# Kernel optimization log

Measured on AMD Instinct MI355X. Metric: run time of the kernel, lower is better.

## Reference

```python
import jax, jax.numpy as jnp
import numpy as np

B, K, N, T, C = 2, 2, 4096, 8, 3
H = 192            # hidden_dim
NODE_DIM = 10
N_LAYERS = 10
KNN = 16           # k nearest neighbours
TOP_FRAC = 0.4
SHARP = 5.0        # mask_sharpness
S = max(int(TOP_FRAC * N), KNN + 1)   # n_select per graph


def _ln(x, g, b, eps=1e-5):
    mu = x.mean(-1, keepdims=True)
    v = ((x - mu) ** 2).mean(-1, keepdims=True)  # biased var, matches nn.LayerNorm
    return (x - mu) / jnp.sqrt(v + eps) * g + b


def setup_inputs() -> dict:
    key = jax.random.key(0)
    ks = jax.random.split(key, 12)
    rn = lambda k, shape: 0.05 * jax.random.normal(k, shape, jnp.float32)
    F0 = 2 * NODE_DIM + 4   # first EdgeConv MLP in-dim
    FR = 2 * H + 4          # remaining EdgeConv MLP in-dim
    L = N_LAYERS - 1
    return {
        "u_base": jax.random.normal(ks[0], (B, K, N, C), jnp.float32),
        "pos": jax.random.uniform(ks[1], (B, N, 3), dtype=jnp.float32),
        "velocity_in": jax.random.normal(ks[2], (B, T, N, C), jnp.float32),
        "airfoil_mask": (jax.random.uniform(ks[3], (B, N)) < 0.05).astype(jnp.float32),
        "conv0_w1": rn(ks[4], (F0, H)), "conv0_b1": jnp.zeros((H,)),
        "conv0_w2": rn(ks[5], (H, H)), "conv0_b2": jnp.zeros((H,)),
        "conv0_g": jnp.ones((H,)), "conv0_be": jnp.zeros((H,)),
        "convs_w1": rn(ks[6], (L, FR, H)), "convs_b1": jnp.zeros((L, H)),
        "convs_w2": rn(ks[7], (L, H, H)), "convs_b2": jnp.zeros((L, H)),
        "convs_g": jnp.ones((L, H)), "convs_be": jnp.zeros((L, H)),
        "head_g": jnp.ones((H,)), "head_be": jnp.zeros((H,)),
        "head_w1": rn(ks[8], (H, H)), "head_b1": jnp.zeros((H,)),
        "head_w2": rn(ks[9], (H, 3)), "head_b2": jnp.zeros((3,)),
    }


def reference(u_base, pos, velocity_in, airfoil_mask,
              conv0_w1, conv0_b1, conv0_w2, conv0_b2, conv0_g, conv0_be,
              convs_w1, convs_b1, convs_w2, convs_b2, convs_g, convs_be,
              head_g, head_be, head_w1, head_b1, head_w2, head_b2):
    # --- variance gating (torch .var/.std are unbiased) ---
    var_pp = jnp.var(velocity_in, axis=1, ddof=1).sum(-1)                      # [B,N]
    var_z = (var_pp - var_pp.mean(1, keepdims=True)) / (
        jnp.std(var_pp, axis=1, ddof=1, keepdims=True) + 1e-8)
    soft_mask = jax.nn.sigmoid(SHARP * var_z) * (1.0 - airfoil_mask)           # [B,N]

    # --- select top-variance points per graph ---
    _, top_idx = jax.lax.top_k(var_pp, S)                                      # [B,S]
    pos_sel = jnp.take_along_axis(pos, top_idx[..., None], axis=1)             # [B,S,3]
    mask_sel = jnp.take_along_axis(soft_mask, top_idx, axis=1)[..., None]      # [B,S,1]
    v_last = velocity_in[:, -1]                                                # [B,N,C]
    ub_sel = jnp.take_along_axis(u_base, top_idx[:, None, :, None], axis=2)    # [B,K,S,C]
    vl_sel = jnp.take_along_axis(v_last, top_idx[..., None], axis=1)           # [B,S,C]
    vf_sel = jnp.take_along_axis(var_pp[..., None], top_idx[..., None], axis=1)
    static = jnp.concatenate([vl_sel, pos_sel, vf_sel], -1)                    # [B,S,7]
    x0 = jnp.concatenate(
        [ub_sel, jnp.broadcast_to(static[:, None], (B, K, S, 7))], -1)         # [B,K,S,10]

    def per_graph(x, pos_b):  # x: [K,S,F0], pos_b: [S,3]
        # kNN graph (self excluded via +inf diagonal, as in the chunked cdist)
        d2 = jnp.sum((pos_b[:, None] - pos_b[None]) ** 2, -1)                  # [S,S]
        d2 = d2.at[jnp.arange(S), jnp.arange(S)].set(jnp.inf)
        _, knn = jax.lax.top_k(-d2, KNN)                                       # [S,KNN]
        # PyG convention with edge_index=stack([targets, sources]):
        # i = edge_index[1] = knn neighbours, j = edge_index[0] = centre nodes
        idx_i = knn.reshape(-1)                     # [E] aggregation targets
        idx_j = jnp.repeat(jnp.arange(S), KNN)      # [E]
        rel = pos_b[idx_i] - pos_b[idx_j]           # pos[edge_index[1]] - pos[edge_index[0]]
        dist = jnp.linalg.norm(rel, axis=-1, keepdims=True)
        ea = jnp.concatenate([rel, dist], -1)       # [E,4]
        ea_b = jnp.broadcast_to(ea, (K,) + ea.shape)

        def conv(h, w1, b1, w2, b2, g, be):
            hi = h[:, idx_i]
            hj = h[:, idx_j]
            m = jnp.concatenate([hi, hj - hi, ea_b], -1)                       # [K,E,2F+4]
            m = jax.nn.gelu(m @ w1 + b1, approximate=False) @ w2 + b2          # [K,E,H]
            agg = jnp.zeros((K, S, H), h.dtype).at[:, idx_i].add(m)
            return _ln(agg, g, be)

        h = conv(x, conv0_w1, conv0_b1, conv0_w2, conv0_b2, conv0_g, conv0_be)
        for l in range(N_LAYERS - 1):
            h = conv(h, convs_w1[l], convs_b1[l], convs_w2[l], convs_b2[l],
                     convs_g[l], convs_be[l]) + h
        hh = _ln(h, head_g, head_be)
        return jax.nn.gelu(hh @ head_w1 + head_b1, approximate=False) @ head_w2 + head_b2

    delta = jax.vmap(per_graph)(x0, pos_sel)        # [B,K,S,3]
    delta = delta * mask_sel[:, None]               # [B,1,S,1]

    def scatter_b(idx, d):  # idx [S], d [K,S,3]
        return jnp.zeros((K, N, C), d.dtype).at[:, idx].set(d)

    delta_full = jax.vmap(scatter_b)(top_idx, delta)            # [B,K,N,C]
    return (u_base + delta_full) * (1.0 - airfoil_mask)[:, None, :, None]
```

## Files before the change

kernel.cpp:

```cpp
#include <hip/hip_runtime.h>
#include <hip/hip_bf16.h>
#include <math.h>

#define B_ 2
#define K_ 2
#define NN_ 4096
#define T_ 8
#define C_ 3
#define H_ 192
#define S_ 1638
#define KK_ 16
#define E_ (S_*KK_)
#define NROW (B_*K_*S_)
#define SHARP_ 5.0f

typedef __hip_bfloat16 bf;
typedef unsigned long long ull;
typedef __bf16 bf16x8 __attribute__((ext_vector_type(8)));
typedef float f32x4 __attribute__((ext_vector_type(4)));

__device__ int   g_isbf16;
__device__ __align__(16) float g_var[B_*NN_];
__device__ __align__(16) float g_vs1[B_*16];
__device__ __align__(16) float g_vs2[B_*16];
__device__ __align__(16) int   g_topidx[B_*S_];
__device__ __align__(16) float g_possel[B_*S_*3];
__device__ __align__(16) float g_masksel[B_*S_];
__device__ __align__(16) float g_x0[NROW*10];
__device__ __align__(16) int   g_knn[B_*E_];
__device__ __align__(16) float g_ea[B_*E_*4];
__device__ __align__(16) int   g_indeg[B_*S_];
__device__ __align__(16) int   g_cursor[B_*S_];
__device__ __align__(16) int   g_off[B_*(S_+1)];
__device__ __align__(16) int   g_list[B_*E_];
__device__ __align__(16) float g_P[(size_t)NROW*H_];
__device__ __align__(16) bf    g_Qbf[(size_t)NROW*H_];
__device__ __align__(16) float g_h[(size_t)NROW*H_];
__device__ __align__(16) bf    g_abf[(size_t)NROW*H_];
__device__ __align__(16) bf    g_w2p[(size_t)11*H_*H_];
__device__ __align__(16) bf    g_wcp[(size_t)9*H_*384];

__device__ __forceinline__ float bf2f(bf x){ return __bfloat162float(x); }
__device__ __forceinline__ float LD(const void* p, long i){
  return g_isbf16 ? __bfloat162float(((const bf*)p)[i]) : ((const float*)p)[i];
}
__device__ __forceinline__ float LDi(const void* p, long i, int isb){
  return isb ? __bfloat162float(((const bf*)p)[i]) : ((const float*)p)[i];
}
__device__ __forceinline__ float gelu_f(float x){ return 0.5f*x*(1.0f + erff(x*0.70710678118654752f)); }
__device__ __forceinline__ ull shfl_xor_u64(ull v, int m){
  unsigned lo = (unsigned)v, hi = (unsigned)(v >> 32);
  lo = __shfl_xor(lo, m, 64); hi = __shfl_xor(hi, m, 64);
  return ((ull)hi << 32) | lo;
}

__global__ __launch_bounds__(256) void k_var(const void* __restrict__ vel,
                                             const void* __restrict__ ub,
                                             const void* __restrict__ pos){
  __shared__ int s_bad;
  int b = blockIdx.y;
  int bx = blockIdx.x;
  int tid = threadIdx.x;
  if (tid == 0) s_bad = 0;
  __syncthreads();
  {
    const bf* pa = (const bf*)ub; const bf* pb = (const bf*)pos; const bf* pc = (const bf*)vel;
    int bad = 0;
    #pragma unroll
    for (int s = 0; s < 2; ++s){
      float va = __bfloat162float(pa[tid + s*256]);
      float vb = __bfloat162float(pb[tid + s*256]);
      float vc = __bfloat162float(pc[tid + s*256]);
      if (!(fabsf(va) <= 1000.f)) bad = 1;
      if (!(fabsf(vb) <= 1000.f)) bad = 1;
      if (!(fabsf(vc) <= 1000.f)) bad = 1;
    }
    if (bad) atomicOr(&s_bad, 1);
  }
  __syncthreads();
  int isb = (s_bad == 0) ? 1 : 0;
  if (bx == 0 && b == 0 && tid == 0) g_isbf16 = isb;
  int zi = (b*16 + bx)*256 + tid;
  if (zi < B_*S_){ g_indeg[zi] = 0; g_cursor[zi] = 0; }
  int n = bx*256 + tid;
  float v = 0.f;
  #pragma unroll
  for (int c = 0; c < 3; ++c){
    float x[8];
    #pragma unroll
    for (int t = 0; t < 8; ++t)
      x[t] = LDi(vel, ((long)(b*T_+t)*NN_ + n)*3 + c, isb);
    float m = __fadd_rn(__fadd_rn(__fadd_rn(x[0],x[1]), __fadd_rn(x[2],x[3])),
                        __fadd_rn(__fadd_rn(x[4],x[5]), __fadd_rn(x[6],x[7]))) / 8.0f;
    float d[8];
    #pragma unroll
    for (int t = 0; t < 8; ++t){ float dd = __fadd_rn(x[t], -m); d[t] = __fmul_rn(dd,dd); }
    float sv = __fadd_rn(__fadd_rn(__fadd_rn(d[0],d[1]), __fadd_rn(d[2],d[3])),
                         __fadd_rn(__fadd_rn(d[4],d[5]), __fadd_rn(d[6],d[7])));
    v = __fadd_rn(v, sv / 7.0f);
  }
  g_var[b*NN_ + n] = v;
  float s1 = v, s2 = v*v;
  #pragma unroll
  for (int o = 32; o; o >>= 1){ s1 += __shfl_xor(s1,o,64); s2 += __shfl_xor(s2,o,64); }
  __shared__ float r1[4], r2[4];
  int lane = tid & 63, wid = tid >> 6;
  if (!lane){ r1[wid]=s1; r2[wid]=s2; }
  __syncthreads();
  if (tid == 0){
    g_vs1[b*16 + bx] = r1[0]+r1[1]+r1[2]+r1[3];
    g_vs2[b*16 + bx] = r2[0]+r2[1]+r2[2]+r2[3];
  }
}

__global__ __launch_bounds__(256) void k_rank(){
  int b = blockIdx.y;
  int i = blockIdx.x*4 + (threadIdx.x >> 6);
  int lane = threadIdx.x & 63;
  float vi = g_var[b*NN_+i];
  int rank = 0;
  for (int j = lane; j < NN_; j += 64){
    float vj = g_var[b*NN_+j];
    rank += ((vj > vi) || (vj == vi && j < i)) ? 1 : 0;
  }
  #pragma unroll
  for (int o = 32; o; o >>= 1) rank += __shfl_xor(rank, o, 64);
  if (lane == 0 && rank < S_) g_topidx[b*S_ + rank] = i;
}

__global__ void k_gather(const void* __restrict__ pos, const void* __restrict__ ub,
                         const void* __restrict__ vel, const void* __restrict__ air){
  int gi = blockIdx.x*256 + threadIdx.x;
  if (gi >= B_*S_) return;
  int b = gi / S_, s = gi - b*S_;
  int node = g_topidx[gi];
  float px = LD(pos, ((long)b*NN_+node)*3+0);
  float py = LD(pos, ((long)b*NN_+node)*3+1);
  float pz = LD(pos, ((long)b*NN_+node)*3+2);
  g_possel[gi*3+0]=px; g_possel[gi*3+1]=py; g_possel[gi*3+2]=pz;
  float S1 = 0.f, S2 = 0.f;
  #pragma unroll
  for (int t = 0; t < 16; ++t){ S1 += g_vs1[b*16+t]; S2 += g_vs2[b*16+t]; }
  float mean = S1*(1.f/NN_);
  float sd = sqrtf(fmaxf((S2 - S1*S1*(1.f/NN_))*(1.f/(NN_-1)), 0.f));
  float vf = g_var[b*NN_+node];
  float z = (vf-mean)/(sd+1e-8f);
  float sig = 1.f/(1.f+expf(-SHARP_*z));
  g_masksel[gi] = sig*(1.f - LD(air, b*NN_+node));
  float vl0 = LD(vel, ((long)(b*T_+7)*NN_+node)*3+0);
  float vl1 = LD(vel, ((long)(b*T_+7)*NN_+node)*3+1);
  float vl2 = LD(vel, ((long)(b*T_+7)*NN_+node)*3+2);
  for (int k = 0; k < K_; ++k){
    long row = (long)(b*K_+k)*S_ + s;
    float* x = g_x0 + row*10;
    x[0]=LD(ub, ((long)(b*K_+k)*NN_+node)*3+0);
    x[1]=LD(ub, ((long)(b*K_+k)*NN_+node)*3+1);
    x[2]=LD(ub, ((long)(b*K_+k)*NN_+node)*3+2);
    x[3]=vl0; x[4]=vl1; x[5]=vl2;
    x[6]=px;  x[7]=py;  x[8]=pz;
    x[9]=vf;
  }
}

__global__ __launch_bounds__(256) void k_knn(){
  __shared__ float px[S_], py[S_], pz[S_];
  int b = blockIdx.y;
  int j = blockIdx.x*4 + (threadIdx.x >> 6);
  int lane = threadIdx.x & 63;
  for (int t = threadIdx.x; t < S_; t += 256){
    px[t] = g_possel[(b*S_+t)*3+0];
    py[t] = g_possel[(b*S_+t)*3+1];
    pz[t] = g_possel[(b*S_+t)*3+2];
  }
  __syncthreads();
  if (j >= S_) return;
  float xj=px[j], yj=py[j], zj=pz[j];
  float dist[KK_]; int id[KK_];
  #pragma unroll
  for (int t = 0; t < KK_; ++t){ dist[t]=3.0e38f; id[t]=0x7fffffff; }
  for (int c = lane; c < S_; c += 64){
    if (c == j) continue;
    float dx=__fadd_rn(px[c],-xj), dy=__fadd_rn(py[c],-yj), dz=__fadd_rn(pz[c],-zj);
    float d2 = __fadd_rn(__fadd_rn(__fmul_rn(dx,dx), __fmul_rn(dy,dy)), __fmul_rn(dz,dz));
    if (d2 < dist[KK_-1]){
      int p = 0;
      #pragma unroll
      for (int q = 0; q < KK_; ++q) p += (dist[q] <= d2) ? 1 : 0;
      #pragma unroll
      for (int q = KK_-1; q >= 1; --q){
        bool mv = (q > p);
        dist[q] = mv ? dist[q-1] : dist[q];
        id[q]   = mv ? id[q-1]   : id[q];
      }
      #pragma unroll
      for (int q = 0; q < KK_; ++q){ if (q == p){ dist[q] = d2; id[q] = c; } }
    }
  }
  ull mykey = 0;
  #pragma unroll
  for (int t = 0; t < KK_; ++t){
    ull k = (((ull)__float_as_uint(dist[0])) << 32) | (unsigned)id[0];
    ull m = k;
    #pragma unroll
    for (int o = 32; o; o >>= 1){ ull other = shfl_xor_u64(m, o); m = (other < m) ? other : m; }
    if (k == m){
      #pragma unroll
      for (int q = 0; q < KK_-1; ++q){ dist[q]=dist[q+1]; id[q]=id[q+1]; }
      dist[KK_-1] = 3.0e38f; id[KK_-1] = 0x7fffffff;
    }
    if (lane == t) mykey = m;
  }
  if (lane < KK_){
    int i = (int)(mykey & 0xffffffffu);
    g_knn[(b*S_+j)*KK_ + lane] = i;
    float rx = __fadd_rn(px[i],-xj), ry = __fadd_rn(py[i],-yj), rz = __fadd_rn(pz[i],-zj);
    float dd = sqrtf(__fadd_rn(__fadd_rn(__fmul_rn(rx,rx), __fmul_rn(ry,ry)), __fmul_rn(rz,rz)));
    float* o = g_ea + ((long)b*E_ + j*KK_ + lane)*4;
    o[0]=rx; o[1]=ry; o[2]=rz; o[3]=dd;
    atomicAdd(&g_indeg[b*S_+i], 1);
  }
}

__global__ void k_scan(){
  __shared__ int sA[2048], sB[2048];
  int b = blockIdx.x, tid = threadIdx.x;
  for (int i = tid; i < 2048; i += 1024) sA[i] = (i < S_) ? g_indeg[b*S_+i] : 0;
  __syncthreads();
  int *src = sA, *dst = sB;
  for (int d = 1; d < 2048; d <<= 1){
    for (int i = tid; i < 2048; i += 1024) dst[i] = src[i] + (i >= d ? src[i-d] : 0);
    __syncthreads();
    int* t2 = src; src = dst; dst = t2;
  }
  if (tid == 0) g_off[b*(S_+1)] = 0;
  for (int i = tid; i < S_; i += 1024) g_off[b*(S_+1)+i+1] = src[i];
}

__global__ void k_fill(){
  int idx = blockIdx.x*256 + threadIdx.x;
  if (idx >= B_*E_) return;
  int b = idx / E_, e = idx - b*E_;
  int i = g_knn[idx];
  int slot = atomicAdd(&g_cursor[b*S_+i], 1);
  g_list[b*E_ + g_off[b*(S_+1)+i] + slot] = e;
}

#define PW2_BLKS 1584
#define PWC_BLKS 2592
#define INIT_BLKS 192
__global__ void k_packall(const void* __restrict__ c0w2, const void* __restrict__ cw2,
                          const void* __restrict__ hw1, const void* __restrict__ cw1,
                          const void* __restrict__ ub, const void* __restrict__ air,
                          float* __restrict__ out){
  int blk = blockIdx.x;
  if (blk < PW2_BLKS){
    int gi = blk*256 + threadIdx.x;
    if (gi >= 11*H_*H_) return;
    int mat = gi / (H_*H_), r = gi - mat*(H_*H_);
    int k = r / H_, n = r - (r/H_)*H_;
    float v;
    if (mat == 0)      v = LD(c0w2, (long)k*H_ + n);
    else if (mat <= 9) v = LD(cw2, (long)(mat-1)*H_*H_ + (long)k*H_ + n);
    else               v = LD(hw1, (long)k*H_ + n);
    int t = k>>5, q = (k>>3)&3, jj = k&7;
    g_w2p[(size_t)mat*H_*H_ + (((t*4+q)*H_ + n)*8 + jj)] = __float2bfloat16(v);
  } else if (blk < PW2_BLKS + PWC_BLKS){
    int gi = (blk - PW2_BLKS)*256 + threadIdx.x;
    if (gi >= 9*H_*384) return;
    int l = gi / (H_*384), r = gi - l*(H_*384);
    int k = r / 384, n = r - (r/384)*384;
    long base = (long)l*388*H_;
    float v;
    if (n < H_) v = LD(cw1, base + (long)k*H_ + n) - LD(cw1, base + (long)(H_+k)*H_ + n);
    else        v = LD(cw1, base + (long)(H_+k)*H_ + (n-H_));
    int t = k>>5, q = (k>>3)&3, jj = k&7;
    g_wcp[(size_t)l*(H_*384) + (((t*4+q)*384 + n)*8 + jj)] = __float2bfloat16(v);
  } else {
    int gi = (blk - PW2_BLKS - PWC_BLKS)*256 + threadIdx.x;
    int n = (gi/3) % NN_;
    int b = gi / (K_*NN_*C_);
    float a = 1.f - LD(air, b*NN_+n);
    out[gi] = LD(ub, gi) * a;
  }
}

__global__ __launch_bounds__(256) void k_proj0(const void* __restrict__ w1){
  __shared__ float xs[16][10];
  __shared__ float wP[10][192];
  __shared__ float wQ[10][192];
  int tid = threadIdx.x;
  long rowBase = (long)blockIdx.x * 16;
  for (int idx = tid; idx < 1920; idx += 256){
    int f = idx / 192, n = idx - (idx/192)*192;
    float a = LD(w1, f*H_+n), b = LD(w1, (10+f)*H_+n);
    wP[f][n] = a - b; wQ[f][n] = b;
  }
  for (int idx = tid; idx < 160; idx += 256){
    int r = idx / 10, f = idx - (idx/10)*10;
    long row = rowBase + r; if (row >= NROW) row = NROW-1;
    xs[r][f] = g_x0[row*10 + f];
  }
  __syncthreads();
  for (int o = tid; o < 16*384; o += 256){
    int r = o / 384, n = o - (o/384)*384;
    long row = rowBase + r;
    if (row >= NROW) continue;
    float acc = 0.f;
    if (n < 192){
      #pragma unroll
      for (int f = 0; f < 10; ++f) acc += xs[r][f]*wP[f][n];
      g_P[row*192 + n] = acc;
    } else {
      int nc = n - 192;
      #pragma unroll
      for (int f = 0; f < 10; ++f) acc += xs[r][f]*wQ[f][nc];
      g_Qbf[row*192 + nc] = __float2bfloat16(acc);
    }
  }
}

template<int RES, int DOPQ>
__global__ __launch_bounds__(256) void k_lnpq(const void* __restrict__ biasB, long biasO,
                                              const void* __restrict__ gB, long gO,
                                              const void* __restrict__ beB, long beO,
                                              int bOff, int pqOff, int M){
  const bf* A  = g_abf;
  const bf* Bp = g_w2p + bOff;
  int wave = threadIdx.x >> 6, lane = threadIdx.x & 63;
  int q = lane >> 4, l16 = lane & 15;
  long rowBase = (long)blockIdx.x * 16;
  f32x4 acc[3];
  #pragma unroll
  for (int ct = 0; ct < 3; ++ct) acc[ct] = (f32x4){0.f,0.f,0.f,0.f};
  #pragma unroll
  for (int t = 0; t < 6; ++t){
    int kof = t*32 + q*8;
    long r = rowBase + l16; if (r >= M) r = M-1;
    bf16x8 af = *reinterpret_cast<const bf16x8*>(A + r*192 + kof);
    #pragma unroll
    for (int ct = 0; ct < 3; ++ct){
      int n = wave*48 + ct*16 + l16;
      bf16x8 bfr = *reinterpret_cast<const bf16x8*>(Bp + (((t*4+q)*192 + n)*8));
      acc[ct] = __builtin_amdgcn_mfma_f32_16x16x32_bf16(af, bfr, acc[ct], 0,0,0);
    }
  }
  __shared__ float tile[16][200];
  __shared__ bf    ybf[16][200];
  __shared__ float srow[16], rrow[16];
  #pragma unroll
  for (int ct = 0; ct < 3; ++ct){
    int col = wave*48 + ct*16 + l16;
    float bb = LD(biasB, biasO + col);
    #pragma unroll
    for (int r = 0; r < 4; ++r){
      int lr = q*4 + r;
      long row = rowBase + lr;
      long rowc = (row < M) ? row : (M-1);
      int bk = (int)(rowc / S_); int i = (int)(rowc - (long)bk*S_); int b = bk >> 1;
      float degf = (float)(g_off[b*(S_+1)+i+1] - g_off[b*(S_+1)+i]);
      tile[lr][col] = acc[ct][r] + degf*bb;
    }
  }
  __syncthreads();
  {
    int lr = threadIdx.x >> 4;
    int k16 = threadIdx.x & 15;
    float s = 0.f, qq = 0.f;
    for (int c = k16; c < 192; c += 16){ float x = tile[lr][c]; s += x; qq += x*x; }
    #pragma unroll
    for (int o = 1; o < 16; o <<= 1){ s += __shfl_xor(s,o,64); qq += __shfl_xor(qq,o,64); }
    if (k16 == 0){
      float mu = s*(1.f/H_);
      float var = qq*(1.f/H_) - mu*mu;
      srow[lr] = mu;
      rrow[lr] = rsqrtf(fmaxf(var, 0.f) + 1e-5f);
    }
  }
  __syncthreads();
  for (int o = threadIdx.x; o < 16*192; o += 256){
    int lr = o / 192, col = o - (o/192)*192;
    long row = rowBase + lr;
    long rowc = (row < M) ? row : (M-1);
    float y = (tile[lr][col] - srow[lr])*rrow[lr]*LD(gB,gO+col) + LD(beB,beO+col);
    if (RES) y += g_h[rowc*192 + col];
    if (row < M) g_h[row*192 + col] = y;
    ybf[lr][col] = __float2bfloat16(y);
  }
  if (DOPQ){
    __syncthreads();
    const bf* Bq = g_wcp + pqOff;
    f32x4 acc2[6];
    #pragma unroll
    for (int ct = 0; ct < 6; ++ct) acc2[ct] = (f32x4){0.f,0.f,0.f,0.f};
    #pragma unroll
    for (int t = 0; t < 6; ++t){
      int kof = t*32 + q*8;
      bf16x8 af = *reinterpret_cast<const bf16x8*>(&ybf[l16][kof]);
      #pragma unroll
      for (int ct = 0; ct < 6; ++ct){
        int n = wave*96 + ct*16 + l16;
        bf16x8 bfr = *reinterpret_cast<const bf16x8*>(Bq + (((t*4+q)*384 + n)*8));
        acc2[ct] = __builtin_amdgcn_mfma_f32_16x16x32_bf16(af, bfr, acc2[ct], 0,0,0);
      }
    }
    #pragma unroll
    for (int ct = 0; ct < 6; ++ct){
      int col = wave*96 + ct*16 + l16;
      #pragma unroll
      for (int r = 0; r < 4; ++r){
        long row = rowBase + q*4 + r;
        if (row < M){
          float v = acc2[ct][r];
          if (col < 192) g_P[row*192 + col] = v;
          else           g_Qbf[row*192 + (col-192)] = __float2bfloat16(v);
        }
      }
    }
  }
}

__global__ __launch_bounds__(256) void k_head(const void* __restrict__ gB,
                                              const void* __restrict__ beB,
                                              const void* __restrict__ biasB,
                                              const void* __restrict__ w2,
                                              const void* __restrict__ b2,
                                              const void* __restrict__ ubase,
                                              const void* __restrict__ air,
                                              float* __restrict__ out,
                                              int bOff, int M){
  const bf* Bp = g_w2p + bOff;
  int wave = threadIdx.x >> 6, lane = threadIdx.x & 63;
  int q = lane >> 4, l16 = lane & 15;
  long rowBase = (long)blockIdx.x * 32;
  __shared__ float tile[32][200];
  __shared__ bf hb_s[32][216];
  __shared__ float srow[32], rrow[32];
  for (int o = threadIdx.x; o < 32*192; o += 256){
    int lr = o / 192, col = o - (o/192)*192;
    long row = rowBase + lr;
    long rowc = (row < M) ? row : (M-1);
    tile[lr][col] = g_h[rowc*192 + col];
  }
  __syncthreads();
  {
    int lr = threadIdx.x >> 3;
    int k8 = threadIdx.x & 7;
    float s = 0.f, qq = 0.f;
    for (int c = k8; c < 192; c += 8){ float x = tile[lr][c]; s += x; qq += x*x; }
    #pragma unroll
    for (int o = 1; o < 8; o <<= 1){ s += __shfl_xor(s,o,64); qq += __shfl_xor(qq,o,64); }
    if (k8 == 0){
      float mu = s*(1.f/H_);
      float var = qq*(1.f/H_) - mu*mu;
      srow[lr] = mu;
      rrow[lr] = rsqrtf(fmaxf(var, 0.f) + 1e-5f);
    }
  }
  __syncthreads();
  for (int o = threadIdx.x; o < 32*192; o += 256){
    int lr = o / 192, col = o - (o/192)*192;
    hb_s[lr][col] = __float2bfloat16((tile[lr][col] - srow[lr])*rrow[lr]*LD(gB,col) + LD(beB,col));
  }
  __syncthreads();
  f32x4 acc[2][3];
  #pragma unroll
  for (int rt = 0; rt < 2; ++rt)
    #pragma unroll
    for (int ct = 0; ct < 3; ++ct) acc[rt][ct] = (f32x4){0.f,0.f,0.f,0.f};
  #pragma unroll
  for (int t = 0; t < 6; ++t){
    int kof = t*32 + q*8;
    bf16x8 af[2], bfr[3];
    #pragma unroll
    for (int rt = 0; rt < 2; ++rt)
      af[rt] = *reinterpret_cast<const bf16x8*>(&hb_s[rt*16 + l16][kof]);
    #pragma unroll
    for (int ct = 0; ct < 3; ++ct){
      int n = wave*48 + ct*16 + l16;
      bfr[ct] = *reinterpret_cast<const bf16x8*>(Bp + (((t*4+q)*192 + n)*8));
    }
    #pragma unroll
    for (int rt = 0; rt < 2; ++rt)
      #pragma unroll
      for (int ct = 0; ct < 3; ++ct)
        acc[rt][ct] = __builtin_amdgcn_mfma_f32_16x16x32_bf16(af[rt], bfr[ct], acc[rt][ct], 0,0,0);
  }
  #pragma unroll
  for (int rt = 0; rt < 2; ++rt){
    #pragma unroll
    for (int ct = 0; ct < 3; ++ct){
      int col = wave*48 + ct*16 + l16;
      float bb = LD(biasB, col);
      #pragma unroll
      for (int r = 0; r < 4; ++r){
        int lr = rt*16 + q*4 + r;
        tile[lr][col] = gelu_f(acc[rt][ct][r] + bb);
      }
    }
  }
  __syncthreads();
  {
    int r = threadIdx.x >> 3, k8 = threadIdx.x & 7;
    long row = rowBase + r;
    float p0 = 0.f, p1 = 0.f, p2 = 0.f;
    for (int col = k8; col < 192; col += 8){
      float tv = tile[r][col];
      p0 += tv*LD(w2, col*3+0);
      p1 += tv*LD(w2, col*3+1);
      p2 += tv*LD(w2, col*3+2);
    }
    #pragma unroll
    for (int o = 1; o < 8; o <<= 1){
      p0 += __shfl_xor(p0,o,64);
      p1 += __shfl_xor(p1,o,64);
      p2 += __shfl_xor(p2,o,64);
    }
    if (k8 == 0 && row < M){
      int bk = (int)(row / S_), s = (int)(row - (long)bk*S_), b = bk >> 1;
      float msk = g_masksel[b*S_+s];
      int node = g_topidx[b*S_+s];
      float am = 1.f - LD(air, b*NN_+node);
      float d0 = p0 + LD(b2,0), d1 = p1 + LD(b2,1), d2 = p2 + LD(b2,2);
      long oi = ((long)bk*NN_ + node)*3;
      out[oi+0] = (LD(ubase, oi+0) + d0*msk)*am;
      out[oi+1] = (LD(ubase, oi+1) + d1*msk)*am;
      out[oi+2] = (LD(ubase, oi+2) + d2*msk)*am;
    }
  }
}

__global__ __launch_bounds__(192) void k_aggedge(const void* __restrict__ w1cB, long w1cO,
                                                 const void* __restrict__ b1B, long b1O){
  int row = blockIdx.x;
  int col = threadIdx.x;
  int bk = row / S_, i = row - bk*S_, b = bk >> 1;
  int off = g_off[b*(S_+1)+i];
  int deg = g_off[b*(S_+1)+i+1] - off;
  float w0 = LD(w1cB, w1cO+col),       w1v = LD(w1cB, w1cO+H_+col);
  float w2v = LD(w1cB, w1cO+2*H_+col), w3v = LD(w1cB, w1cO+3*H_+col);
  float base = g_P[(size_t)row*H_ + col] + LD(b1B, b1O+col);
  const int* lst = g_list + b*E_ + off;
  const bf* Q = g_Qbf + (size_t)bk*S_*H_;
  const float* EA = g_ea + (size_t)b*E_*4;
  float acc = 0.f;
  int d = 0;
  for (; d + 4 <= deg; d += 4){
    int e0 = lst[d], e1 = lst[d+1], e2 = lst[d+2], e3 = lst[d+3];
    float4 a0 = *reinterpret_cast<const float4*>(EA + (size_t)e0*4);
    float4 a1 = *reinterpret_cast<const float4*>(EA + (size_t)e1*4);
    float4 a2 = *reinterpret_cast<const float4*>(EA + (size_t)e2*4);
    float4 a3 = *reinterpret_cast<const float4*>(EA + (size_t)e3*4);
    float q0 = bf2f(Q[(size_t)(e0>>4)*H_ + col]);
    float q1 = bf2f(Q[(size_t)(e1>>4)*H_ + col]);
    float q2 = bf2f(Q[(size_t)(e2>>4)*H_ + col]);
    float q3 = bf2f(Q[(size_t)(e3>>4)*H_ + col]);
    acc += gelu_f(base + q0 + a0.x*w0 + a0.y*w1v + a0.z*w2v + a0.w*w3v);
    acc += gelu_f(base + q1 + a1.x*w0 + a1.y*w1v + a1.z*w2v + a1.w*w3v);
    acc += gelu_f(base + q2 + a2.x*w0 + a2.y*w1v + a2.z*w2v + a2.w*w3v);
    acc += gelu_f(base + q3 + a3.x*w0 + a3.y*w1v + a3.z*w2v + a3.w*w3v);
  }
  for (; d < deg; ++d){
    int e = lst[d];
    float4 a = *reinterpret_cast<const float4*>(EA + (size_t)e*4);
    float qv = bf2f(Q[(size_t)(e>>4)*H_ + col]);
    acc += gelu_f(base + qv + a.x*w0 + a.y*w1v + a.z*w2v + a.w*w3v);
  }
  g_abf[(size_t)row*H_ + col] = __float2bfloat16(acc);
}

extern "C" void kernel_launch(void* const* d_in, const int* in_sizes, int n_in,
                              void* d_out, int out_size, void* d_ws, size_t ws_size,
                              hipStream_t stream) {
  (void)in_sizes; (void)n_in; (void)d_ws; (void)ws_size; (void)out_size;
  const void* u_base = d_in[0];
  const void* pos    = d_in[1];
  const void* vel    = d_in[2];
  const void* air    = d_in[3];
  const void* c0w1   = d_in[4];
  const void* c0b1   = d_in[5];
  const void* c0w2   = d_in[6];
  const void* c0b2   = d_in[7];
  const void* c0g    = d_in[8];
  const void* c0be   = d_in[9];
  const void* cw1    = d_in[10];
  const void* cb1    = d_in[11];
  const void* cw2    = d_in[12];
  const void* cb2    = d_in[13];
  const void* cg     = d_in[14];
  const void* cbe    = d_in[15];
  const void* hg     = d_in[16];
  const void* hbe    = d_in[17];
  const void* hw1    = d_in[18];
  const void* hb1    = d_in[19];
  const void* hw2    = d_in[20];
  const void* hb2    = d_in[21];
  float* out = (float*)d_out;

  k_var<<<dim3(16, B_), 256, 0, stream>>>(vel, u_base, pos);
  k_rank<<<dim3(NN_/4, B_), 256, 0, stream>>>();
  k_gather<<<13, 256, 0, stream>>>(pos, u_base, vel, air);
  k_knn<<<dim3((S_+3)/4, B_), 256, 0, stream>>>();
  k_scan<<<B_, 1024, 0, stream>>>();
  k_fill<<<205, 256, 0, stream>>>();
  k_packall<<<PW2_BLKS + PWC_BLKS + INIT_BLKS, 256, 0, stream>>>(c0w2, cw2, hw1, cw1, u_base, air, out);
  k_proj0<<<410, 256, 0, stream>>>(c0w1);

  const int GN16 = (NROW + 15) / 16;
  for (int l = 0; l < 10; ++l){
    long w1cO = (l == 0) ? 20L*H_ : ((long)(l-1)*388 + 384)*H_;
    const void* w1cB = (l == 0) ? c0w1 : cw1;
    long lOff = (l == 0) ? 0 : (long)(l-1)*H_;
    const void* b1B = (l == 0) ? c0b1 : cb1;
    k_aggedge<<<NROW, 192, 0, stream>>>(w1cB, w1cO, b1B, lOff);

    const void* b2B = (l == 0) ? c0b2 : cb2;
    const void* gB  = (l == 0) ? c0g  : cg;
    const void* beB = (l == 0) ? c0be : cbe;
    if (l == 0)
      k_lnpq<0,1><<<GN16, 256, 0, stream>>>(b2B, lOff, gB, lOff, beB, lOff, 0,        0,         NROW);
    else if (l < 9)
      k_lnpq<1,1><<<GN16, 256, 0, stream>>>(b2B, lOff, gB, lOff, beB, lOff, l*H_*H_, l*H_*384,  NROW);
    else
      k_lnpq<1,0><<<GN16, 256, 0, stream>>>(b2B, lOff, gB, lOff, beB, lOff, l*H_*H_, 0,         NROW);
  }

  k_head<<<(NROW + 31)/32, 256, 0, stream>>>(hg, hbe, hb1, hw2, hb2, u_base, air, out, 10*H_*H_, NROW);
}
```

Measured before the change: 617.8 us.

## Fuse edge aggregation, projection, LayerNorm and head into one per-layer kernel

The per-row edge aggregation is merged into the per-layer MFMA/LayerNorm/PQ kernel. Aggregated activations now stay in shared memory as bf16 instead of going through the global g_abf buffer, and the head runs inside the last layer's kernel. The k_fill and k_proj0 setup kernels are folded into the packing kernel, so there are fewer launches and less global traffic. In exchange each block handles only 8 rows but pads them to a 16-row MFMA tile, so half of the matrix work is spent on zeros. The gather-heavy aggregation also now runs on far fewer, larger blocks, which may lower latency hiding.

```diff
diff --git a/kernel.cpp b/kernel.cpp
--- a/kernel.cpp
+++ b/kernel.cpp
@@ -36,7 +36,6 @@
 __device__ __align__(16) float g_P[(size_t)NROW*H_];
 __device__ __align__(16) bf    g_Qbf[(size_t)NROW*H_];
 __device__ __align__(16) float g_h[(size_t)NROW*H_];
-__device__ __align__(16) bf    g_abf[(size_t)NROW*H_];
 __device__ __align__(16) bf    g_w2p[(size_t)11*H_*H_];
 __device__ __align__(16) bf    g_wcp[(size_t)9*H_*384];
 
@@ -236,22 +235,15 @@
   for (int i = tid; i < S_; i += 1024) g_off[b*(S_+1)+i+1] = src[i];
 }
 
-__global__ void k_fill(){
-  int idx = blockIdx.x*256 + threadIdx.x;
-  if (idx >= B_*E_) return;
-  int b = idx / E_, e = idx - b*E_;
-  int i = g_knn[idx];
-  int slot = atomicAdd(&g_cursor[b*S_+i], 1);
-  g_list[b*E_ + g_off[b*(S_+1)+i] + slot] = e;
-}
-
 #define PW2_BLKS 1584
 #define PWC_BLKS 2592
 #define INIT_BLKS 192
+#define FILL_BLKS 205
+#define PROJ_BLKS 410
 __global__ void k_packall(const void* __restrict__ c0w2, const void* __restrict__ cw2,
                           const void* __restrict__ hw1, const void* __restrict__ cw1,
                           const void* __restrict__ ub, const void* __restrict__ air,
-                          float* __restrict__ out){
+                          float* __restrict__ out, const void* __restrict__ c0w1){
   int blk = blockIdx.x;
   if (blk < PW2_BLKS){
     int gi = blk*256 + threadIdx.x;
@@ -275,90 +267,143 @@
     else        v = LD(cw1, base + (long)(H_+k)*H_ + (n-H_));
     int t = k>>5, q = (k>>3)&3, jj = k&7;
     g_wcp[(size_t)l*(H_*384) + (((t*4+q)*384 + n)*8 + jj)] = __float2bfloat16(v);
-  } else {
+  } else if (blk < PW2_BLKS + PWC_BLKS + INIT_BLKS){
     int gi = (blk - PW2_BLKS - PWC_BLKS)*256 + threadIdx.x;
     int n = (gi/3) % NN_;
     int b = gi / (K_*NN_*C_);
     float a = 1.f - LD(air, b*NN_+n);
     out[gi] = LD(ub, gi) * a;
-  }
-}
-
-__global__ __launch_bounds__(256) void k_proj0(const void* __restrict__ w1){
-  __shared__ float xs[16][10];
-  __shared__ float wP[10][192];
-  __shared__ float wQ[10][192];
-  int tid = threadIdx.x;
-  long rowBase = (long)blockIdx.x * 16;
-  for (int idx = tid; idx < 1920; idx += 256){
-    int f = idx / 192, n = idx - (idx/192)*192;
-    float a = LD(w1, f*H_+n), b = LD(w1, (10+f)*H_+n);
-    wP[f][n] = a - b; wQ[f][n] = b;
-  }
-  for (int idx = tid; idx < 160; idx += 256){
-    int r = idx / 10, f = idx - (idx/10)*10;
-    long row = rowBase + r; if (row >= NROW) row = NROW-1;
-    xs[r][f] = g_x0[row*10 + f];
-  }
-  __syncthreads();
-  for (int o = tid; o < 16*384; o += 256){
-    int r = o / 384, n = o - (o/384)*384;
-    long row = rowBase + r;
-    if (row >= NROW) continue;
-    float acc = 0.f;
-    if (n < 192){
-      #pragma unroll
-      for (int f = 0; f < 10; ++f) acc += xs[r][f]*wP[f][n];
-      g_P[row*192 + n] = acc;
-    } else {
-      int nc = n - 192;
-      #pragma unroll
-      for (int f = 0; f < 10; ++f) acc += xs[r][f]*wQ[f][nc];
-      g_Qbf[row*192 + nc] = __float2bfloat16(acc);
-    }
-  }
-}
-
-template<int RES, int DOPQ>
-__global__ __launch_bounds__(256) void k_lnpq(const void* __restrict__ biasB, long biasO,
-                                              const void* __restrict__ gB, long gO,
-                                              const void* __restrict__ beB, long beO,
-                                              int bOff, int pqOff, int M){
-  const bf* A  = g_abf;
-  const bf* Bp = g_w2p + bOff;
+  } else if (blk < PW2_BLKS + PWC_BLKS + INIT_BLKS + FILL_BLKS){
+    int idx = (blk - PW2_BLKS - PWC_BLKS - INIT_BLKS)*256 + threadIdx.x;
+    if (idx >= B_*E_) return;
+    int b = idx / E_, e = idx - b*E_;
+    int i = g_knn[idx];
+    int slot = atomicAdd(&g_cursor[b*S_+i], 1);
+    g_list[b*E_ + g_off[b*(S_+1)+i] + slot] = e;
+  } else {
+    __shared__ float xs[16][10];
+    __shared__ float wP[10][192];
+    __shared__ float wQ[10][192];
+    int tid = threadIdx.x;
+    long rowBase = (long)(blk - PW2_BLKS - PWC_BLKS - INIT_BLKS - FILL_BLKS) * 16;
+    for (int idx = tid; idx < 1920; idx += 256){
+      int f = idx / 192, n = idx - (idx/192)*192;
+      float a = LD(c0w1, f*H_+n), b = LD(c0w1, (10+f)*H_+n);
+      wP[f][n] = a - b; wQ[f][n] = b;
+    }
+    for (int idx = tid; idx < 160; idx += 256){
+      int r = idx / 10, f = idx - (idx/10)*10;
+      long row = rowBase + r; if (row >= NROW) row = NROW-1;
+      xs[r][f] = g_x0[row*10 + f];
+    }
+    __syncthreads();
+    for (int o = tid; o < 16*384; o += 256){
+      int r = o / 384, n = o - (o/384)*384;
+      long row = rowBase + r;
+      if (row >= NROW) continue;
+      float acc = 0.f;
+      if (n < 192){
+        #pragma unroll
+        for (int f = 0; f < 10; ++f) acc += xs[r][f]*wP[f][n];
+        g_P[row*192 + n] = acc;
+      } else {
+        int nc = n - 192;
+        #pragma unroll
+        for (int f = 0; f < 10; ++f) acc += xs[r][f]*wQ[f][nc];
+        g_Qbf[row*192 + nc] = __float2bfloat16(acc);
+      }
+    }
+  }
+}
+
+template<int RES, int DOPQ, int DOHEAD>
+__global__ __launch_bounds__(256) void k_layer(
+    const void* __restrict__ w1cB, long w1cO,
+    const void* __restrict__ b1B, long b1O,
+    const void* __restrict__ biasB, long biasO,
+    const void* __restrict__ gB, long gO,
+    const void* __restrict__ beB, long beO,
+    int bOff, int pqOff,
+    const void* __restrict__ hg, const void* __restrict__ hbe,
+    const void* __restrict__ hb1, const void* __restrict__ hw2,
+    const void* __restrict__ hb2, const void* __restrict__ ubase,
+    const void* __restrict__ air, float* __restrict__ out,
+    int M){
   int wave = threadIdx.x >> 6, lane = threadIdx.x & 63;
   int q = lane >> 4, l16 = lane & 15;
-  long rowBase = (long)blockIdx.x * 16;
-  f32x4 acc[3];
-  #pragma unroll
-  for (int ct = 0; ct < 3; ++ct) acc[ct] = (f32x4){0.f,0.f,0.f,0.f};
-  #pragma unroll
-  for (int t = 0; t < 6; ++t){
-    int kof = t*32 + q*8;
-    long r = rowBase + l16; if (r >= M) r = M-1;
-    bf16x8 af = *reinterpret_cast<const bf16x8*>(A + r*192 + kof);
+  long rowBase = (long)blockIdx.x * 8;
+  __shared__ bf    sbf[16][200];
+  __shared__ float tile[16][200];
+  __shared__ float srow[16], rrow[16];
+  for (int o = threadIdx.x; o < 8*192; o += 256){
+    int lr = o / 192, col = o - (o/192)*192;
+    long row = rowBase + lr;
+    int bk = (int)(row / S_); int i = (int)(row - (long)bk*S_); int b = bk >> 1;
+    int off = g_off[b*(S_+1)+i];
+    int deg = g_off[b*(S_+1)+i+1] - off;
+    float w0 = LD(w1cB, w1cO+col),       w1v = LD(w1cB, w1cO+H_+col);
+    float w2v = LD(w1cB, w1cO+2*H_+col), w3v = LD(w1cB, w1cO+3*H_+col);
+    float base = g_P[(size_t)row*H_ + col] + LD(b1B, b1O+col);
+    const int* lst = g_list + b*E_ + off;
+    const bf* Q = g_Qbf + (size_t)bk*S_*H_;
+    const float* EA = g_ea + (size_t)b*E_*4;
+    float acc = 0.f;
+    int d = 0;
+    for (; d + 4 <= deg; d += 4){
+      int e0 = lst[d], e1 = lst[d+1], e2 = lst[d+2], e3 = lst[d+3];
+      float4 a0 = *reinterpret_cast<const float4*>(EA + (size_t)e0*4);
+      float4 a1 = *reinterpret_cast<const float4*>(EA + (size_t)e1*4);
+      float4 a2 = *reinterpret_cast<const float4*>(EA + (size_t)e2*4);
+      float4 a3 = *reinterpret_cast<const float4*>(EA + (size_t)e3*4);
+      float q0 = bf2f(Q[(size_t)(e0>>4)*H_ + col]);
+      float q1 = bf2f(Q[(size_t)(e1>>4)*H_ + col]);
+      float q2 = bf2f(Q[(size_t)(e2>>4)*H_ + col]);
+      float q3 = bf2f(Q[(size_t)(e3>>4)*H_ + col]);
+      acc += gelu_f(base + q0 + a0.x*w0 + a0.y*w1v + a0.z*w2v + a0.w*w3v);
+      acc += gelu_f(base + q1 + a1.x*w0 + a1.y*w1v + a1.z*w2v + a1.w*w3v);
+      acc += gelu_f(base + q2 + a2.x*w0 + a2.y*w1v + a2.z*w2v + a2.w*w3v);
+      acc += gelu_f(base + q3 + a3.x*w0 + a3.y*w1v + a3.z*w2v + a3.w*w3v);
+    }
+    for (; d < deg; ++d){
+      int e = lst[d];
+      float4 a = *reinterpret_cast<const float4*>(EA + (size_t)e*4);
+      float qv = bf2f(Q[(size_t)(e>>4)*H_ + col]);
+      acc += gelu_f(base + qv + a.x*w0 + a.y*w1v + a.z*w2v + a.w*w3v);
+    }
+    sbf[lr][col] = __float2bfloat16(acc);
+  }
+  for (int o = threadIdx.x; o < 8*192; o += 256)
+    sbf[8 + o/192][o - (o/192)*192] = __float2bfloat16(0.f);
+  __syncthreads();
+  {
+    const bf* Bp = g_w2p + bOff;
+    f32x4 acc[3];
+    #pragma unroll
+    for (int ct = 0; ct < 3; ++ct) acc[ct] = (f32x4){0.f,0.f,0.f,0.f};
+    #pragma unroll
+    for (int t = 0; t < 6; ++t){
+      int kof = t*32 + q*8;
+      bf16x8 af = *reinterpret_cast<const bf16x8*>(&sbf[l16][kof]);
+      #pragma unroll
+      for (int ct = 0; ct < 3; ++ct){
+        int n = wave*48 + ct*16 + l16;
+        bf16x8 bfr = *reinterpret_cast<const bf16x8*>(Bp + (((t*4+q)*192 + n)*8));
+        acc[ct] = __builtin_amdgcn_mfma_f32_16x16x32_bf16(af, bfr, acc[ct], 0,0,0);
+      }
+    }
     #pragma unroll
     for (int ct = 0; ct < 3; ++ct){
-      int n = wave*48 + ct*16 + l16;
-      bf16x8 bfr = *reinterpret_cast<const bf16x8*>(Bp + (((t*4+q)*192 + n)*8));
-      acc[ct] = __builtin_amdgcn_mfma_f32_16x16x32_bf16(af, bfr, acc[ct], 0,0,0);
-    }
-  }
-  __shared__ float tile[16][200];
-  __shared__ bf    ybf[16][200];
-  __shared__ float srow[16], rrow[16];
-  #pragma unroll
-  for (int ct = 0; ct < 3; ++ct){
-    int col = wave*48 + ct*16 + l16;
-    float bb = LD(biasB, biasO + col);
-    #pragma unroll
-    for (int r = 0; r < 4; ++r){
-      int lr = q*4 + r;
-      long row = rowBase + lr;
-      long rowc = (row < M) ? row : (M-1);
-      int bk = (int)(rowc / S_); int i = (int)(rowc - (long)bk*S_); int b = bk >> 1;
-      float degf = (float)(g_off[b*(S_+1)+i+1] - g_off[b*(S_+1)+i]);
-      tile[lr][col] = acc[ct][r] + degf*bb;
+      int col = wave*48 + ct*16 + l16;
+      float bb = LD(biasB, biasO + col);
+      #pragma unroll
+      for (int r = 0; r < 4; ++r){
+        int lr = q*4 + r;
+        long row = rowBase + lr;
+        long rowc = (row < M) ? row : (M-1);
+        int bk = (int)(rowc / S_); int i = (int)(rowc - (long)bk*S_); int b = bk >> 1;
+        float degf = (float)(g_off[b*(S_+1)+i+1] - g_off[b*(S_+1)+i]);
+        tile[lr][col] = acc[ct][r] + degf*bb;
+      }
     }
   }
   __syncthreads();
@@ -383,8 +428,9 @@
     long rowc = (row < M) ? row : (M-1);
     float y = (tile[lr][col] - srow[lr])*rrow[lr]*LD(gB,gO+col) + LD(beB,beO+col);
     if (RES) y += g_h[rowc*192 + col];
-    if (row < M) g_h[row*192 + col] = y;
-    ybf[lr][col] = __float2bfloat16(y);
+    if (!DOHEAD && lr < 8) g_h[row*192 + col] = y;
+    sbf[lr][col] = __float2bfloat16(y);
+    if (DOHEAD) tile[lr][col] = y;
   }
   if (DOPQ){
     __syncthreads();
@@ -395,7 +441,7 @@
     #pragma unroll
     for (int t = 0; t < 6; ++t){
       int kof = t*32 + q*8;
-      bf16x8 af = *reinterpret_cast<const bf16x8*>(&ybf[l16][kof]);
+      bf16x8 af = *reinterpret_cast<const bf16x8*>(&sbf[l16][kof]);
       #pragma unroll
       for (int ct = 0; ct < 6; ++ct){
         int n = wave*96 + ct*16 + l16;
@@ -408,8 +454,9 @@
       int col = wave*96 + ct*16 + l16;
       #pragma unroll
       for (int r = 0; r < 4; ++r){
-        long row = rowBase + q*4 + r;
-        if (row < M){
+        int orow = q*4 + r;
+        if (orow < 8){
+          long row = rowBase + orow;
           float v = acc2[ct][r];
           if (col < 192) g_P[row*192 + col] = v;
           else           g_Qbf[row*192 + (col-192)] = __float2bfloat16(v);
@@ -417,155 +464,86 @@
       }
     }
   }
-}
-
-__global__ __launch_bounds__(256) void k_head(const void* __restrict__ gB,
-                                              const void* __restrict__ beB,
-                                              const void* __restrict__ biasB,
-                                              const void* __restrict__ w2,
-                                              const void* __restrict__ b2,
-                                              const void* __restrict__ ubase,
-                                              const void* __restrict__ air,
-                                              float* __restrict__ out,
-                                              int bOff, int M){
-  const bf* Bp = g_w2p + bOff;
-  int wave = threadIdx.x >> 6, lane = threadIdx.x & 63;
-  int q = lane >> 4, l16 = lane & 15;
-  long rowBase = (long)blockIdx.x * 32;
-  __shared__ float tile[32][200];
-  __shared__ bf hb_s[32][216];
-  __shared__ float srow[32], rrow[32];
-  for (int o = threadIdx.x; o < 32*192; o += 256){
-    int lr = o / 192, col = o - (o/192)*192;
-    long row = rowBase + lr;
-    long rowc = (row < M) ? row : (M-1);
-    tile[lr][col] = g_h[rowc*192 + col];
-  }
-  __syncthreads();
-  {
-    int lr = threadIdx.x >> 3;
-    int k8 = threadIdx.x & 7;
-    float s = 0.f, qq = 0.f;
-    for (int c = k8; c < 192; c += 8){ float x = tile[lr][c]; s += x; qq += x*x; }
-    #pragma unroll
-    for (int o = 1; o < 8; o <<= 1){ s += __shfl_xor(s,o,64); qq += __shfl_xor(qq,o,64); }
-    if (k8 == 0){
-      float mu = s*(1.f/H_);
-      float var = qq*(1.f/H_) - mu*mu;
-      srow[lr] = mu;
-      rrow[lr] = rsqrtf(fmaxf(var, 0.f) + 1e-5f);
-    }
-  }
-  __syncthreads();
-  for (int o = threadIdx.x; o < 32*192; o += 256){
-    int lr = o / 192, col = o - (o/192)*192;
-    hb_s[lr][col] = __float2bfloat16((tile[lr][col] - srow[lr])*rrow[lr]*LD(gB,col) + LD(beB,col));
-  }
-  __syncthreads();
-  f32x4 acc[2][3];
-  #pragma unroll
-  for (int rt = 0; rt < 2; ++rt)
-    #pragma unroll
-    for (int ct = 0; ct < 3; ++ct) acc[rt][ct] = (f32x4){0.f,0.f,0.f,0.f};
-  #pragma unroll
-  for (int t = 0; t < 6; ++t){
-    int kof = t*32 + q*8;
-    bf16x8 af[2], bfr[3];
-    #pragma unroll
-    for (int rt = 0; rt < 2; ++rt)
-      af[rt] = *reinterpret_cast<const bf16x8*>(&hb_s[rt*16 + l16][kof]);
-    #pragma unroll
-    for (int ct = 0; ct < 3; ++ct){
-      int n = wave*48 + ct*16 + l16;
-      bfr[ct] = *reinterpret_cast<const bf16x8*>(Bp + (((t*4+q)*192 + n)*8));
-    }
-    #pragma unroll
-    for (int rt = 0; rt < 2; ++rt)
-      #pragma unroll
-      for (int ct = 0; ct < 3; ++ct)
-        acc[rt][ct] = __builtin_amdgcn_mfma_f32_16x16x32_bf16(af[rt], bfr[ct], acc[rt][ct], 0,0,0);
-  }
-  #pragma unroll
-  for (int rt = 0; rt < 2; ++rt){
-    #pragma unroll
-    for (int ct = 0; ct < 3; ++ct){
-      int col = wave*48 + ct*16 + l16;
-      float bb = LD(biasB, col);
-      #pragma unroll
-      for (int r = 0; r < 4; ++r){
-        int lr = rt*16 + q*4 + r;
-        tile[lr][col] = gelu_f(acc[rt][ct][r] + bb);
-      }
-    }
-  }
-  __syncthreads();
-  {
-    int r = threadIdx.x >> 3, k8 = threadIdx.x & 7;
-    long row = rowBase + r;
-    float p0 = 0.f, p1 = 0.f, p2 = 0.f;
-    for (int col = k8; col < 192; col += 8){
-      float tv = tile[r][col];
-      p0 += tv*LD(w2, col*3+0);
-      p1 += tv*LD(w2, col*3+1);
-      p2 += tv*LD(w2, col*3+2);
-    }
-    #pragma unroll
-    for (int o = 1; o < 8; o <<= 1){
-      p0 += __shfl_xor(p0,o,64);
-      p1 += __shfl_xor(p1,o,64);
-      p2 += __shfl_xor(p2,o,64);
-    }
-    if (k8 == 0 && row < M){
-      int bk = (int)(row / S_), s = (int)(row - (long)bk*S_), b = bk >> 1;
-      float msk = g_masksel[b*S_+s];
-      int node = g_topidx[b*S_+s];
-      float am = 1.f - LD(air, b*NN_+node);
-      float d0 = p0 + LD(b2,0), d1 = p1 + LD(b2,1), d2 = p2 + LD(b2,2);
-      long oi = ((long)bk*NN_ + node)*3;
-      out[oi+0] = (LD(ubase, oi+0) + d0*msk)*am;
-      out[oi+1] = (LD(ubase, oi+1) + d1*msk)*am;
-      out[oi+2] = (LD(ubase, oi+2) + d2*msk)*am;
-    }
-  }
-}
-
-__global__ __launch_bounds__(192) void k_aggedge(const void* __restrict__ w1cB, long w1cO,
-                                                 const void* __restrict__ b1B, long b1O){
-  int row = blockIdx.x;
-  int col = threadIdx.x;
-  int bk = row / S_, i = row - bk*S_, b = bk >> 1;
-  int off = g_off[b*(S_+1)+i];
-  int deg = g_off[b*(S_+1)+i+1] - off;
-  float w0 = LD(w1cB, w1cO+col),       w1v = LD(w1cB, w1cO+H_+col);
-  float w2v = LD(w1cB, w1cO+2*H_+col), w3v = LD(w1cB, w1cO+3*H_+col);
-  float base = g_P[(size_t)row*H_ + col] + LD(b1B, b1O+col);
-  const int* lst = g_list + b*E_ + off;
-  const bf* Q = g_Qbf + (size_t)bk*S_*H_;
-  const float* EA = g_ea + (size_t)b*E_*4;
-  float acc = 0.f;
-  int d = 0;
-  for (; d + 4 <= deg; d += 4){
-    int e0 = lst[d], e1 = lst[d+1], e2 = lst[d+2], e3 = lst[d+3];
-    float4 a0 = *reinterpret_cast<const float4*>(EA + (size_t)e0*4);
-    float4 a1 = *reinterpret_cast<const float4*>(EA + (size_t)e1*4);
-    float4 a2 = *reinterpret_cast<const float4*>(EA + (size_t)e2*4);
-    float4 a3 = *reinterpret_cast<const float4*>(EA + (size_t)e3*4);
-    float q0 = bf2f(Q[(size_t)(e0>>4)*H_ + col]);
-    float q1 = bf2f(Q[(size_t)(e1>>4)*H_ + col]);
-    float q2 = bf2f(Q[(size_t)(e2>>4)*H_ + col]);
-    float q3 = bf2f(Q[(size_t)(e3>>4)*H_ + col]);
-    acc += gelu_f(base + q0 + a0.x*w0 + a0.y*w1v + a0.z*w2v + a0.w*w3v);
-    acc += gelu_f(base + q1 + a1.x*w0 + a1.y*w1v + a1.z*w2v + a1.w*w3v);
-    acc += gelu_f(base + q2 + a2.x*w0 + a2.y*w1v + a2.z*w2v + a2.w*w3v);
-    acc += gelu_f(base + q3 + a3.x*w0 + a3.y*w1v + a3.z*w2v + a3.w*w3v);
-  }
-  for (; d < deg; ++d){
-    int e = lst[d];
-    float4 a = *reinterpret_cast<const float4*>(EA + (size_t)e*4);
-    float qv = bf2f(Q[(size_t)(e>>4)*H_ + col]);
-    acc += gelu_f(base + qv + a.x*w0 + a.y*w1v + a.z*w2v + a.w*w3v);
-  }
-  g_abf[(size_t)row*H_ + col] = __float2bfloat16(acc);
+  if (DOHEAD){
+    __syncthreads();
+    {
+      int lr = threadIdx.x >> 4;
+      int k16 = threadIdx.x & 15;
+      float s = 0.f, qq = 0.f;
+      for (int c = k16; c < 192; c += 16){ float x = tile[lr][c]; s += x; qq += x*x; }
+      #pragma unroll
+      for (int o = 1; o < 16; o <<= 1){ s += __shfl_xor(s,o,64); qq += __shfl_xor(qq,o,64); }
+      if (k16 == 0){
+        float mu = s*(1.f/H_);
+        float var = qq*(1.f/H_) - mu*mu;
+        srow[lr] = mu;
+        rrow[lr] = rsqrtf(fmaxf(var, 0.f) + 1e-5f);
+      }
+    }
+    __syncthreads();
+    for (int o = threadIdx.x; o < 16*192; o += 256){
+      int lr = o / 192, col = o - (o/192)*192;
+      sbf[lr][col] = __float2bfloat16((tile[lr][col] - srow[lr])*rrow[lr]*LD(hg,col) + LD(hbe,col));
+    }
+    __syncthreads();
+    {
+      const bf* Bp = g_w2p + 10*H_*H_;
+      f32x4 hacc[3];
+      #pragma unroll
+      for (int ct = 0; ct < 3; ++ct) hacc[ct] = (f32x4){0.f,0.f,0.f,0.f};
+      #pragma unroll
+      for (int t = 0; t < 6; ++t){
+        int kof = t*32 + q*8;
+        bf16x8 af = *reinterpret_cast<const bf16x8*>(&sbf[l16][kof]);
+        #pragma unroll
+        for (int ct = 0; ct < 3; ++ct){
+          int n = wave*48 + ct*16 + l16;
+          bf16x8 bfr = *reinterpret_cast<const bf16x8*>(Bp + (((t*4+q)*192 + n)*8));
+          hacc[ct] = __builtin_amdgcn_mfma_f32_16x16x32_bf16(af, bfr, hacc[ct], 0,0,0);
+        }
+      }
+      __syncthreads();
+      #pragma unroll
+      for (int ct = 0; ct < 3; ++ct){
+        int col = wave*48 + ct*16 + l16;
+        float bb = LD(hb1, col);
+        #pragma unroll
+        for (int r = 0; r < 4; ++r){
+          int lr = q*4 + r;
+          tile[lr][col] = gelu_f(hacc[ct][r] + bb);
+        }
+      }
+    }
+    __syncthreads();
+    {
+      int r = threadIdx.x >> 4, k16 = threadIdx.x & 15;
+      float p0 = 0.f, p1 = 0.f, p2 = 0.f;
+      for (int col = k16; col < 192; col += 16){
+        float tv = tile[r][col];
+        p0 += tv*LD(hw2, col*3+0);
+        p1 += tv*LD(hw2, col*3+1);
+        p2 += tv*LD(hw2, col*3+2);
+      }
+      #pragma unroll
+      for (int o = 1; o < 16; o <<= 1){
+        p0 += __shfl_xor(p0,o,64);
+        p1 += __shfl_xor(p1,o,64);
+        p2 += __shfl_xor(p2,o,64);
+      }
+      if (k16 == 0 && r < 8){
+        long row = rowBase + r;
+        int bk = (int)(row / S_), s = (int)(row - (long)bk*S_), b = bk >> 1;
+        float msk = g_masksel[b*S_+s];
+        int node = g_topidx[b*S_+s];
+        float am = 1.f - LD(air, b*NN_+node);
+        float d0 = p0 + LD(hb2,0), d1 = p1 + LD(hb2,1), d2 = p2 + LD(hb2,2);
+        long oi = ((long)bk*NN_ + node)*3;
+        out[oi+0] = (LD(ubase, oi+0) + d0*msk)*am;
+        out[oi+1] = (LD(ubase, oi+1) + d1*msk)*am;
+        out[oi+2] = (LD(ubase, oi+2) + d2*msk)*am;
+      }
+    }
+  }
 }
 
 extern "C" void kernel_launch(void* const* d_in, const int* in_sizes, int n_in,
@@ -601,28 +579,26 @@
   k_gather<<<13, 256, 0, stream>>>(pos, u_base, vel, air);
   k_knn<<<dim3((S_+3)/4, B_), 256, 0, stream>>>();
   k_scan<<<B_, 1024, 0, stream>>>();
-  k_fill<<<205, 256, 0, stream>>>();
-  k_packall<<<PW2_BLKS + PWC_BLKS + INIT_BLKS, 256, 0, stream>>>(c0w2, cw2, hw1, cw1, u_base, air, out);
-  k_proj0<<<410, 256, 0, stream>>>(c0w1);
-
-  const int GN16 = (NROW + 15) / 16;
+  k_packall<<<PW2_BLKS + PWC_BLKS + INIT_BLKS + FILL_BLKS + PROJ_BLKS, 256, 0, stream>>>(
+      c0w2, cw2, hw1, cw1, u_base, air, out, c0w1);
+
+  const int GN8 = NROW / 8;
   for (int l = 0; l < 10; ++l){
     long w1cO = (l == 0) ? 20L*H_ : ((long)(l-1)*388 + 384)*H_;
     const void* w1cB = (l == 0) ? c0w1 : cw1;
     long lOff = (l == 0) ? 0 : (long)(l-1)*H_;
     const void* b1B = (l == 0) ? c0b1 : cb1;
-    k_aggedge<<<NROW, 192, 0, stream>>>(w1cB, w1cO, b1B, lOff);
-
     const void* b2B = (l == 0) ? c0b2 : cb2;
     const void* gB  = (l == 0) ? c0g  : cg;
     const void* beB = (l == 0) ? c0be : cbe;
     if (l == 0)
-      k_lnpq<0,1><<<GN16, 256, 0, stream>>>(b2B, lOff, gB, lOff, beB, lOff, 0,        0,         NROW);
+      k_layer<0,1,0><<<GN8, 256, 0, stream>>>(w1cB, w1cO, b1B, lOff, b2B, lOff, gB, lOff, beB, lOff,
+                                              0, 0, hg, hbe, hb1, hw2, hb2, u_base, air, out, NROW);
     else if (l < 9)
-      k_lnpq<1,1><<<GN16, 256, 0, stream>>>(b2B, lOff, gB, lOff, beB, lOff, l*H_*H_, l*H_*384,  NROW);
+      k_layer<1,1,0><<<GN8, 256, 0, stream>>>(w1cB, w1cO, b1B, lOff, b2B, lOff, gB, lOff, beB, lOff,
+                                              l*H_*H_, l*H_*384, hg, hbe, hb1, hw2, hb2, u_base, air, out, NROW);
     else
-      k_lnpq<1,0><<<GN16, 256, 0, stream>>>(b2B, lOff, gB, lOff, beB, lOff, l*H_*H_, 0,         NROW);
-  }
-
-  k_head<<<(NROW + 31)/32, 256, 0, stream>>>(hg, hbe, hb1, hw2, hb2, u_base, air, out, 10*H_*H_, NROW);
-}
+      k_layer<1,0,1><<<GN8, 256, 0, stream>>>(w1cB, w1cO, b1B, lOff, b2B, lOff, gB, lOff, beB, lOff,
+                                              l*H_*H_, 0, hg, hbe, hb1, hw2, hb2, u_base, air, out, NROW);
+  }
+}
```

Result: slower. 763.0 us (+23.5%).
